# Optimization experiments

Hardware: AMD Instinct MI355X
Metric: run time of the kernel (lower is better)

## Reference

```python
import jax, jax.numpy as jnp
import numpy as np

NEG_INF = -1e9  # matches torch masked_fill value -1000000000.0


def setup_inputs() -> dict:
    key = jax.random.key(0)
    ks = jax.random.split(key, 7)
    B, S = 16, 4096
    scale = 1.0 / np.sqrt(S)  # keep linear outputs O(1) like torch init
    return {
        "x": jax.random.normal(ks[0], (B, S), dtype=jnp.float32),
        "Wq": jax.random.normal(ks[1], (S, S), dtype=jnp.float32) * scale,
        "bq": jax.random.normal(ks[2], (S,), dtype=jnp.float32) * scale,
        "Wk": jax.random.normal(ks[3], (S, S), dtype=jnp.float32) * scale,
        "bk": jax.random.normal(ks[4], (S,), dtype=jnp.float32) * scale,
        "Wv": jax.random.normal(ks[5], (S, S), dtype=jnp.float32) * scale,
        "bv": jax.random.normal(ks[6], (S,), dtype=jnp.float32) * scale,
    }


def reference(x, Wq, bq, Wk, bk, Wv, bv):
    # x: [B, S]; torch Linear: y = x @ W.T + b with W [out, in]
    q = x @ Wq.T + bq  # [B, S]
    k = x @ Wk.T + bk  # [B, S]
    v = x @ Wv.T + bv  # [B, S]
    # d=1 attention: scores[b,i,j] = q[b,i] * k[b,j]  -> outer product
    scores = q[:, :, None] * k[:, None, :]  # [B, S, S]
    S = x.shape[1]
    causal = jnp.tril(jnp.ones((S, S), dtype=bool))  # mask=True path
    scores = jnp.where(causal, scores, NEG_INF)
    attn = jax.nn.softmax(scores, axis=-1)  # [B, S, S]
    out = jnp.einsum("bij,bj->bi", attn, v)  # [B, S]
    return out
```

## Files before the change

### kernel.cpp

```cpp
#include <hip/hip_runtime.h>
#include <math.h>

#define S 4096
#define B 16
#define SC 256
#define R 8

__global__ __launch_bounds__(256) void qkv_kernel(
    const float* __restrict__ x,
    const float* __restrict__ Wq, const float* __restrict__ bq,
    const float* __restrict__ Wk, const float* __restrict__ bk,
    const float* __restrict__ Wv, const float* __restrict__ bv,
    float* __restrict__ q, float* __restrict__ k, float* __restrict__ v)
{
    __shared__ float xs[B][SC];
    const int tid  = threadIdx.x;
    const int lane = tid & 63;
    const int wave = tid >> 6;
    const int bx   = blockIdx.x;
    const int mat  = bx >> 9;
    const int og   = bx & 511;

    const float* W    = (mat == 0) ? Wq : (mat == 1) ? Wk : Wv;
    const float* bias = (mat == 0) ? bq : (mat == 1) ? bk : bv;
    float*       out  = (mat == 0) ? q  : (mat == 1) ? k  : v;
    const int o0  = og * 8 + (wave >> 1) * 4;
    const int bb0 = (wave & 1) * 8;
    const float* Wp = W + (size_t)o0 * S;

    float acc[4][8];
    #pragma unroll
    for (int r = 0; r < 4; ++r)
        #pragma unroll
        for (int bi = 0; bi < 8; ++bi) acc[r][bi] = 0.f;

    #pragma unroll 1
    for (int c = 0; c < S / SC; ++c) {
        __syncthreads();
        #pragma unroll
        for (int r = 0; r < (B * SC / 4) / 256; ++r) {
            int f4 = tid + r * 256;
            int b  = f4 >> 6;
            int s4 = f4 & 63;
            *(float4*)&xs[b][s4 * 4] =
                *(const float4*)&x[(size_t)b * S + c * SC + s4 * 4];
        }
        __syncthreads();
        const int sg = c * SC + lane * 4;
        float4 w0 = *(const float4*)&Wp[0 * S + sg];
        float4 w1 = *(const float4*)&Wp[1 * S + sg];
        float4 w2 = *(const float4*)&Wp[2 * S + sg];
        float4 w3 = *(const float4*)&Wp[3 * S + sg];
        #pragma unroll
        for (int bi = 0; bi < 8; ++bi) {
            float4 xv = *(const float4*)&xs[bb0 + bi][lane * 4];
            acc[0][bi] = fmaf(w0.x, xv.x, acc[0][bi]);
            acc[0][bi] = fmaf(w0.y, xv.y, acc[0][bi]);
            acc[0][bi] = fmaf(w0.z, xv.z, acc[0][bi]);
            acc[0][bi] = fmaf(w0.w, xv.w, acc[0][bi]);
            acc[1][bi] = fmaf(w1.x, xv.x, acc[1][bi]);
            acc[1][bi] = fmaf(w1.y, xv.y, acc[1][bi]);
            acc[1][bi] = fmaf(w1.z, xv.z, acc[1][bi]);
            acc[1][bi] = fmaf(w1.w, xv.w, acc[1][bi]);
            acc[2][bi] = fmaf(w2.x, xv.x, acc[2][bi]);
            acc[2][bi] = fmaf(w2.y, xv.y, acc[2][bi]);
            acc[2][bi] = fmaf(w2.z, xv.z, acc[2][bi]);
            acc[2][bi] = fmaf(w2.w, xv.w, acc[2][bi]);
            acc[3][bi] = fmaf(w3.x, xv.x, acc[3][bi]);
            acc[3][bi] = fmaf(w3.y, xv.y, acc[3][bi]);
            acc[3][bi] = fmaf(w3.z, xv.z, acc[3][bi]);
            acc[3][bi] = fmaf(w3.w, xv.w, acc[3][bi]);
        }
    }

    #pragma unroll
    for (int r = 0; r < 4; ++r) {
        #pragma unroll
        for (int bi = 0; bi < 8; ++bi) {
            float s = acc[r][bi];
            #pragma unroll
            for (int off = 32; off; off >>= 1) s += __shfl_xor(s, off, 64);
            if (lane == r * 8 + bi)
                out[(size_t)(bb0 + bi) * S + o0 + r] = s + bias[o0 + r];
        }
    }
}

__global__ __launch_bounds__(256) void scan_kernel(
    const float* __restrict__ k,
    float* __restrict__ rmax, float* __restrict__ rmin)
{
    __shared__ float smax[256], smin[256];
    const int b = blockIdx.x, t = threadIdx.x;
    const float* kb = k + b * S;

    float seg[16];
    float lmax = -INFINITY, lmin = INFINITY;
    #pragma unroll
    for (int e = 0; e < 16; ++e) {
        seg[e] = kb[t * 16 + e];
        lmax = fmaxf(lmax, seg[e]);
        lmin = fminf(lmin, seg[e]);
    }
    smax[t] = lmax; smin[t] = lmin;
    __syncthreads();
    for (int off = 1; off < 256; off <<= 1) {
        float vx = (t >= off) ? smax[t - off] : -INFINITY;
        float vn = (t >= off) ? smin[t - off] :  INFINITY;
        __syncthreads();
        smax[t] = fmaxf(smax[t], vx);
        smin[t] = fminf(smin[t], vn);
        __syncthreads();
    }
    float runmax = (t > 0) ? smax[t - 1] : -INFINITY;
    float runmin = (t > 0) ? smin[t - 1] :  INFINITY;
    #pragma unroll
    for (int e = 0; e < 16; ++e) {
        runmax = fmaxf(runmax, seg[e]);
        runmin = fminf(runmin, seg[e]);
        rmax[b * S + t * 16 + e] = runmax;
        rmin[b * S + t * 16 + e] = runmin;
    }
}

__global__ __launch_bounds__(256) void attn_kernel(
    const float* __restrict__ q, const float* __restrict__ k,
    const float* __restrict__ v,
    const float* __restrict__ rmax, const float* __restrict__ rmin,
    float* __restrict__ out)
{
    const int tid = threadIdx.x, lane = tid & 63, wave = tid >> 6;
    const int task = blockIdx.x * 4 + wave;
    const int b    = task & 15;
    const int rbi  = task >> 4;
    const int i0   = (511 - rbi) * R;
    const float* kb = k + b * S;
    const float* vb = v + b * S;
    const float LOG2E = 1.4426950408889634f;

    float a[R], cc[R], den[R], num[R];
    #pragma unroll
    for (int r = 0; r < R; ++r) {
        float qi = q[b * S + i0 + r];
        float m  = (qi >= 0.f) ? qi * rmax[b * S + i0 + r]
                               : qi * rmin[b * S + i0 + r];
        a[r]  = qi * LOG2E;
        cc[r] = -m * LOG2E;
        den[r] = 0.f; num[r] = 0.f;
    }

    const int nfull = (i0 + 1) >> 8;
    #pragma unroll 1
    for (int it = 0; it < nfull; ++it) {
        const int j = it * 256 + lane * 4;
        float4 k4 = *(const float4*)&kb[j];
        float4 v4 = *(const float4*)&vb[j];
        #pragma unroll
        for (int jj = 0; jj < 4; ++jj) {
            float kx = (&k4.x)[jj], vx = (&v4.x)[jj];
            #pragma unroll
            for (int r = 0; r < R; ++r) {
                float e = exp2f(fmaf(a[r], kx, cc[r]));
                den[r] += e;
                num[r] = fmaf(e, vx, num[r]);
            }
        }
    }
    const int imax = i0 + R - 1;
    for (int j = nfull * 256 + lane; j <= imax; j += 64) {
        float kx = kb[j], vx = vb[j];
        #pragma unroll
        for (int r = 0; r < R; ++r) {
            float e = (j <= i0 + r) ? exp2f(fmaf(a[r], kx, cc[r])) : 0.f;
            den[r] += e;
            num[r] = fmaf(e, vx, num[r]);
        }
    }

    #pragma unroll
    for (int r = 0; r < R; ++r) {
        float d = den[r], n = num[r];
        #pragma unroll
        for (int off = 32; off; off >>= 1) {
            d += __shfl_xor(d, off, 64);
            n += __shfl_xor(n, off, 64);
        }
        if (lane == r) out[b * S + i0 + r] = n / d;
    }
}

extern "C" void kernel_launch(void* const* d_in, const int* in_sizes, int n_in,
                              void* d_out, int out_size, void* d_ws, size_t ws_size,
                              hipStream_t stream) {
    const float* x  = (const float*)d_in[0];
    const float* Wq = (const float*)d_in[1];
    const float* bq = (const float*)d_in[2];
    const float* Wk = (const float*)d_in[3];
    const float* bk = (const float*)d_in[4];
    const float* Wv = (const float*)d_in[5];
    const float* bv = (const float*)d_in[6];
    float* out = (float*)d_out;

    float* ws   = (float*)d_ws;
    float* q    = ws;
    float* k    = ws + 65536;
    float* v    = ws + 131072;
    float* rmax = ws + 196608;
    float* rmin = ws + 262144;

    qkv_kernel<<<1536, 256, 0, stream>>>(x, Wq, bq, Wk, bk, Wv, bv, q, k, v);
    scan_kernel<<<16, 256, 0, stream>>>(k, rmax, rmin);
    attn_kernel<<<2048, 256, 0, stream>>>(q, k, v, rmax, rmin, out);
}
```

Measured before the change: 104.0 us.

## Drop LDS staging of x and double-buffer W loads in QKV projection

```diff
diff --git a/kernel.cpp b/kernel.cpp
--- a/kernel.cpp
+++ b/kernel.cpp
@@ -3,17 +3,15 @@
 
 #define S 4096
 #define B 16
-#define SC 256
 #define R 8
 
-__global__ __launch_bounds__(256) void qkv_kernel(
+__global__ __launch_bounds__(256, 4) void qkv_kernel(
     const float* __restrict__ x,
     const float* __restrict__ Wq, const float* __restrict__ bq,
     const float* __restrict__ Wk, const float* __restrict__ bk,
     const float* __restrict__ Wv, const float* __restrict__ bv,
     float* __restrict__ q, float* __restrict__ k, float* __restrict__ v)
 {
-    __shared__ float xs[B][SC];
     const int tid  = threadIdx.x;
     const int lane = tid & 63;
     const int wave = tid >> 6;
@@ -26,7 +24,8 @@
     float*       out  = (mat == 0) ? q  : (mat == 1) ? k  : v;
     const int o0  = og * 8 + (wave >> 1) * 4;
     const int bb0 = (wave & 1) * 8;
-    const float* Wp = W + (size_t)o0 * S;
+    const float* Wp = W + (size_t)o0 * S + lane * 4;
+    const float* xp = x + (size_t)bb0 * S + lane * 4;
 
     float acc[4][8];
     #pragma unroll
@@ -34,44 +33,52 @@
         #pragma unroll
         for (int bi = 0; bi < 8; ++bi) acc[r][bi] = 0.f;
 
+    float4 wa0 = *(const float4*)&Wp[0 * S];
+    float4 wa1 = *(const float4*)&Wp[1 * S];
+    float4 wa2 = *(const float4*)&Wp[2 * S];
+    float4 wa3 = *(const float4*)&Wp[3 * S];
+
+#define QKV_COMPUTE(c, W0, W1, W2, W3)                                   \
+    {                                                                    \
+        const int sl = (c) * 256;                                        \
+        _Pragma("unroll")                                                \
+        for (int bi = 0; bi < 8; ++bi) {                                 \
+            float4 xv = *(const float4*)&xp[(size_t)bi * S + sl];        \
+            acc[0][bi] = fmaf(W0.x, xv.x, acc[0][bi]);                   \
+            acc[0][bi] = fmaf(W0.y, xv.y, acc[0][bi]);                   \
+            acc[0][bi] = fmaf(W0.z, xv.z, acc[0][bi]);                   \
+            acc[0][bi] = fmaf(W0.w, xv.w, acc[0][bi]);                   \
+            acc[1][bi] = fmaf(W1.x, xv.x, acc[1][bi]);                   \
+            acc[1][bi] = fmaf(W1.y, xv.y, acc[1][bi]);                   \
+            acc[1][bi] = fmaf(W1.z, xv.z, acc[1][bi]);                   \
+            acc[1][bi] = fmaf(W1.w, xv.w, acc[1][bi]);                   \
+            acc[2][bi] = fmaf(W2.x, xv.x, acc[2][bi]);                   \
+            acc[2][bi] = fmaf(W2.y, xv.y, acc[2][bi]);                   \
+            acc[2][bi] = fmaf(W2.z, xv.z, acc[2][bi]);                   \
+            acc[2][bi] = fmaf(W2.w, xv.w, acc[2][bi]);                   \
+            acc[3][bi] = fmaf(W3.x, xv.x, acc[3][bi]);                   \
+            acc[3][bi] = fmaf(W3.y, xv.y, acc[3][bi]);                   \
+            acc[3][bi] = fmaf(W3.z, xv.z, acc[3][bi]);                   \
+            acc[3][bi] = fmaf(W3.w, xv.w, acc[3][bi]);                   \
+        }                                                                \
+    }
+
     #pragma unroll 1
-    for (int c = 0; c < S / SC; ++c) {
-        __syncthreads();
-        #pragma unroll
-        for (int r = 0; r < (B * SC / 4) / 256; ++r) {
-            int f4 = tid + r * 256;
-            int b  = f4 >> 6;
-            int s4 = f4 & 63;
-            *(float4*)&xs[b][s4 * 4] =
-                *(const float4*)&x[(size_t)b * S + c * SC + s4 * 4];
-        }
-        __syncthreads();
-        const int sg = c * SC + lane * 4;
-        float4 w0 = *(const float4*)&Wp[0 * S + sg];
-        float4 w1 = *(const float4*)&Wp[1 * S + sg];
-        float4 w2 = *(const float4*)&Wp[2 * S + sg];
-        float4 w3 = *(const float4*)&Wp[3 * S + sg];
-        #pragma unroll
-        for (int bi = 0; bi < 8; ++bi) {
-            float4 xv = *(const float4*)&xs[bb0 + bi][lane * 4];
-            acc[0][bi] = fmaf(w0.x, xv.x, acc[0][bi]);
-            acc[0][bi] = fmaf(w0.y, xv.y, acc[0][bi]);
-            acc[0][bi] = fmaf(w0.z, xv.z, acc[0][bi]);
-            acc[0][bi] = fmaf(w0.w, xv.w, acc[0][bi]);
-            acc[1][bi] = fmaf(w1.x, xv.x, acc[1][bi]);
-            acc[1][bi] = fmaf(w1.y, xv.y, acc[1][bi]);
-            acc[1][bi] = fmaf(w1.z, xv.z, acc[1][bi]);
-            acc[1][bi] = fmaf(w1.w, xv.w, acc[1][bi]);
-            acc[2][bi] = fmaf(w2.x, xv.x, acc[2][bi]);
-            acc[2][bi] = fmaf(w2.y, xv.y, acc[2][bi]);
-            acc[2][bi] = fmaf(w2.z, xv.z, acc[2][bi]);
-            acc[2][bi] = fmaf(w2.w, xv.w, acc[2][bi]);
-            acc[3][bi] = fmaf(w3.x, xv.x, acc[3][bi]);
-            acc[3][bi] = fmaf(w3.y, xv.y, acc[3][bi]);
-            acc[3][bi] = fmaf(w3.z, xv.z, acc[3][bi]);
-            acc[3][bi] = fmaf(w3.w, xv.w, acc[3][bi]);
-        }
-    }
+    for (int cc = 0; cc < 8; ++cc) {
+        const int c0 = 2 * cc;
+        float4 wb0 = *(const float4*)&Wp[0 * S + (c0 + 1) * 256];
+        float4 wb1 = *(const float4*)&Wp[1 * S + (c0 + 1) * 256];
+        float4 wb2 = *(const float4*)&Wp[2 * S + (c0 + 1) * 256];
+        float4 wb3 = *(const float4*)&Wp[3 * S + (c0 + 1) * 256];
+        QKV_COMPUTE(c0, wa0, wa1, wa2, wa3);
+        const int cn = (c0 + 2 < 16) ? (c0 + 2) : 15;
+        wa0 = *(const float4*)&Wp[0 * S + cn * 256];
+        wa1 = *(const float4*)&Wp[1 * S + cn * 256];
+        wa2 = *(const float4*)&Wp[2 * S + cn * 256];
+        wa3 = *(const float4*)&Wp[3 * S + cn * 256];
+        QKV_COMPUTE(c0 + 1, wb0, wb1, wb2, wb3);
+    }
+#undef QKV_COMPUTE
 
     #pragma unroll
     for (int r = 0; r < 4; ++r) {
```

Result: slower. 109.6 us (+5.4%).

## Drop LDS staging in QKV GEMV, read x directly with staggered chunk order

Applied to the files above, without the earlier changes.

```diff
diff --git a/kernel.cpp b/kernel.cpp
--- a/kernel.cpp
+++ b/kernel.cpp
@@ -3,7 +3,6 @@
 
 #define S 4096
 #define B 16
-#define SC 256
 #define R 8
 
 __global__ __launch_bounds__(256) void qkv_kernel(
@@ -13,7 +12,6 @@
     const float* __restrict__ Wv, const float* __restrict__ bv,
     float* __restrict__ q, float* __restrict__ k, float* __restrict__ v)
 {
-    __shared__ float xs[B][SC];
     const int tid  = threadIdx.x;
     const int lane = tid & 63;
     const int wave = tid >> 6;
@@ -24,64 +22,78 @@
     const float* W    = (mat == 0) ? Wq : (mat == 1) ? Wk : Wv;
     const float* bias = (mat == 0) ? bq : (mat == 1) ? bk : bv;
     float*       out  = (mat == 0) ? q  : (mat == 1) ? k  : v;
-    const int o0  = og * 8 + (wave >> 1) * 4;
-    const int bb0 = (wave & 1) * 8;
-    const float* Wp = W + (size_t)o0 * S;
-
-    float acc[4][8];
-    #pragma unroll
-    for (int r = 0; r < 4; ++r)
-        #pragma unroll
-        for (int bi = 0; bi < 8; ++bi) acc[r][bi] = 0.f;
+    const int o0 = og * 8 + wave * 2;
+    const float* w0p = W + (size_t)o0 * S + lane * 4;
+    const float* w1p = w0p + S;
+    const float* xp  = x + lane * 4;
+
+    const int cstart = ((og * 5) + mat) & 15;
+
+    float acc[2][16];
+    #pragma unroll
+    for (int r = 0; r < 2; ++r)
+        #pragma unroll
+        for (int b = 0; b < 16; ++b) acc[r][b] = 0.f;
 
     #pragma unroll 1
-    for (int c = 0; c < S / SC; ++c) {
-        __syncthreads();
-        #pragma unroll
-        for (int r = 0; r < (B * SC / 4) / 256; ++r) {
-            int f4 = tid + r * 256;
-            int b  = f4 >> 6;
-            int s4 = f4 & 63;
-            *(float4*)&xs[b][s4 * 4] =
-                *(const float4*)&x[(size_t)b * S + c * SC + s4 * 4];
-        }
-        __syncthreads();
-        const int sg = c * SC + lane * 4;
-        float4 w0 = *(const float4*)&Wp[0 * S + sg];
-        float4 w1 = *(const float4*)&Wp[1 * S + sg];
-        float4 w2 = *(const float4*)&Wp[2 * S + sg];
-        float4 w3 = *(const float4*)&Wp[3 * S + sg];
-        #pragma unroll
-        for (int bi = 0; bi < 8; ++bi) {
-            float4 xv = *(const float4*)&xs[bb0 + bi][lane * 4];
-            acc[0][bi] = fmaf(w0.x, xv.x, acc[0][bi]);
-            acc[0][bi] = fmaf(w0.y, xv.y, acc[0][bi]);
-            acc[0][bi] = fmaf(w0.z, xv.z, acc[0][bi]);
-            acc[0][bi] = fmaf(w0.w, xv.w, acc[0][bi]);
-            acc[1][bi] = fmaf(w1.x, xv.x, acc[1][bi]);
-            acc[1][bi] = fmaf(w1.y, xv.y, acc[1][bi]);
-            acc[1][bi] = fmaf(w1.z, xv.z, acc[1][bi]);
-            acc[1][bi] = fmaf(w1.w, xv.w, acc[1][bi]);
-            acc[2][bi] = fmaf(w2.x, xv.x, acc[2][bi]);
-            acc[2][bi] = fmaf(w2.y, xv.y, acc[2][bi]);
-            acc[2][bi] = fmaf(w2.z, xv.z, acc[2][bi]);
-            acc[2][bi] = fmaf(w2.w, xv.w, acc[2][bi]);
-            acc[3][bi] = fmaf(w3.x, xv.x, acc[3][bi]);
-            acc[3][bi] = fmaf(w3.y, xv.y, acc[3][bi]);
-            acc[3][bi] = fmaf(w3.z, xv.z, acc[3][bi]);
-            acc[3][bi] = fmaf(w3.w, xv.w, acc[3][bi]);
-        }
-    }
-
-    #pragma unroll
-    for (int r = 0; r < 4; ++r) {
-        #pragma unroll
-        for (int bi = 0; bi < 8; ++bi) {
-            float s = acc[r][bi];
+    for (int ccc = 0; ccc < 16; ++ccc) {
+        const int c   = (cstart + ccc) & 15;
+        const int off = c * 256;
+        float4 w0 = *(const float4*)&w0p[off];
+        float4 w1 = *(const float4*)&w1p[off];
+        float4 xa0 = *(const float4*)&xp[(size_t) 0 * S + off];
+        float4 xa1 = *(const float4*)&xp[(size_t) 1 * S + off];
+        float4 xa2 = *(const float4*)&xp[(size_t) 2 * S + off];
+        float4 xa3 = *(const float4*)&xp[(size_t) 3 * S + off];
+        float4 xa4 = *(const float4*)&xp[(size_t) 4 * S + off];
+        float4 xa5 = *(const float4*)&xp[(size_t) 5 * S + off];
+        float4 xa6 = *(const float4*)&xp[(size_t) 6 * S + off];
+        float4 xa7 = *(const float4*)&xp[(size_t) 7 * S + off];
+
+        #define FMA4(r, b, wv, xv)                       \
+            acc[r][b] = fmaf(wv.x, xv.x, acc[r][b]);     \
+            acc[r][b] = fmaf(wv.y, xv.y, acc[r][b]);     \
+            acc[r][b] = fmaf(wv.z, xv.z, acc[r][b]);     \
+            acc[r][b] = fmaf(wv.w, xv.w, acc[r][b]);
+
+        FMA4(0, 0, w0, xa0)  FMA4(1, 0, w1, xa0)
+        FMA4(0, 1, w0, xa1)  FMA4(1, 1, w1, xa1)
+        FMA4(0, 2, w0, xa2)  FMA4(1, 2, w1, xa2)
+        FMA4(0, 3, w0, xa3)  FMA4(1, 3, w1, xa3)
+        FMA4(0, 4, w0, xa4)  FMA4(1, 4, w1, xa4)
+        FMA4(0, 5, w0, xa5)  FMA4(1, 5, w1, xa5)
+        FMA4(0, 6, w0, xa6)  FMA4(1, 6, w1, xa6)
+        FMA4(0, 7, w0, xa7)  FMA4(1, 7, w1, xa7)
+
+        float4 xb0 = *(const float4*)&xp[(size_t) 8 * S + off];
+        float4 xb1 = *(const float4*)&xp[(size_t) 9 * S + off];
+        float4 xb2 = *(const float4*)&xp[(size_t)10 * S + off];
+        float4 xb3 = *(const float4*)&xp[(size_t)11 * S + off];
+        float4 xb4 = *(const float4*)&xp[(size_t)12 * S + off];
+        float4 xb5 = *(const float4*)&xp[(size_t)13 * S + off];
+        float4 xb6 = *(const float4*)&xp[(size_t)14 * S + off];
+        float4 xb7 = *(const float4*)&xp[(size_t)15 * S + off];
+
+        FMA4(0,  8, w0, xb0)  FMA4(1,  8, w1, xb0)
+        FMA4(0,  9, w0, xb1)  FMA4(1,  9, w1, xb1)
+        FMA4(0, 10, w0, xb2)  FMA4(1, 10, w1, xb2)
+        FMA4(0, 11, w0, xb3)  FMA4(1, 11, w1, xb3)
+        FMA4(0, 12, w0, xb4)  FMA4(1, 12, w1, xb4)
+        FMA4(0, 13, w0, xb5)  FMA4(1, 13, w1, xb5)
+        FMA4(0, 14, w0, xb6)  FMA4(1, 14, w1, xb6)
+        FMA4(0, 15, w0, xb7)  FMA4(1, 15, w1, xb7)
+        #undef FMA4
+    }
+
+    #pragma unroll
+    for (int r = 0; r < 2; ++r) {
+        #pragma unroll
+        for (int b = 0; b < 16; ++b) {
+            float s = acc[r][b];
             #pragma unroll
             for (int off = 32; off; off >>= 1) s += __shfl_xor(s, off, 64);
-            if (lane == r * 8 + bi)
-                out[(size_t)(bb0 + bi) * S + o0 + r] = s + bias[o0 + r];
+            if (lane == r * 16 + b)
+                out[(size_t)b * S + o0 + r] = s + bias[o0 + r];
         }
     }
 }
```

Result: slower. 116.4 us (+11.9%).
